# Optimization experiments

Measured on AMD Instinct MI355X. Metric: run time of the kernel, lower is better.

The kernel has to match this reference:

```python
import jax, jax.numpy as jnp
import numpy as np

B, S, D = 2, 400, 512  # batch, seq (src == tgt for self-attention), dim; attn_hidden=0 so d == D


def setup_inputs() -> dict:
    key = jax.random.key(0)
    ks = jax.random.split(key, 9)
    inv = 1.0 / np.sqrt(D)
    return {
        "input": jax.random.normal(ks[0], (B, S, D), jnp.float32),
        "memory_bank": jax.random.normal(ks[1], (B, S, D), jnp.float32),
        # lengths in [S//2, S], guaranteed >= 2 so no row is fully masked
        "memory_lengths": jax.random.randint(ks[2], (B,), S // 2, S + 1, jnp.int32),
        "Wq": jax.random.normal(ks[3], (D, D), jnp.float32) * inv,   # linear_query.weight^T
        "bq": jax.random.normal(ks[4], (D,), jnp.float32) * inv,      # linear_query.bias
        "Wc": jax.random.normal(ks[5], (D, D), jnp.float32) * inv,   # linear_context.weight^T
        "v": jax.random.normal(ks[6], (D,), jnp.float32) * inv,       # v.weight (d -> 1)
        "Wout": jax.random.normal(ks[7], (2 * D, D), jnp.float32) * inv,  # linear_out.weight^T
        "bout": jax.random.normal(ks[8], (D,), jnp.float32) * inv,
    }


def reference(input, memory_bank, memory_lengths, Wq, bq, Wc, v, Wout, bout):
    b, s, d = memory_bank.shape
    # Bahdanau/mlp score: v^T tanh(Wq q + b + Wc h)
    wq = jnp.einsum("btd,de->bte", input, Wq) + bq            # [B,T,d]
    uh = jnp.einsum("bsd,de->bse", memory_bank, Wc)           # [B,S,d]
    wquh = jnp.tanh(wq[:, :, None, :] + uh[:, None, :, :])    # [B,T,S,d] big intermediate
    scores = jnp.einsum("btse,e->bts", wquh, v)               # [B,T,S]
    # padding mask (j < length) with self position masked out on the diagonal
    pos = jnp.arange(s)
    key_mask = pos[None, :] < memory_lengths[:, None]         # [B,S]
    mask = key_mask[:, None, :] & (pos[:, None] != pos[None, :])  # [B,T,S]
    scores = jnp.where(mask, scores, -jnp.inf)
    align = jax.nn.softmax(scores, axis=2)                    # [B,T,S]
    c = jnp.einsum("bts,bsd->btd", align, memory_bank)        # context [B,T,D]
    concat_c = jnp.concatenate([c, input], axis=2)            # [B,T,2D]
    attn_h = jnp.einsum("btf,fd->btd", concat_c, Wout) + bout # [B,T,D]
    # mlp variant: no sigmoid gating
    return attn_h.transpose(1, 0, 2), align.transpose(1, 0, 2)  # [T,B,D], [T,B,S]
```

## Files before the change

kernel.cpp:

```cpp
#include <hip/hip_runtime.h>
#include <math.h>

#define BB 2
#define SS 400
#define DD 512
#define TWO_LOG2E 2.8853900817779268f

#if __has_builtin(__builtin_amdgcn_exp2f)
#define EXP2F(x) __builtin_amdgcn_exp2f(x)
#else
#define EXP2F(x) exp2f(x)
#endif
#define RCPF(x) __builtin_amdgcn_rcpf(x)

#define EAOFF 0
#define MOFF 409600
#define EB4OFF 819200
#define XOFF 1228800

typedef __bf16 bf16x8 __attribute__((ext_vector_type(8)));
typedef float floatx16 __attribute__((ext_vector_type(16)));

__global__ __launch_bounds__(256) void k0_prep(
    const float* __restrict__ Wq, const float* __restrict__ Wc,
    const float* __restrict__ Wout, unsigned short* __restrict__ wt)
{
    const int k0 = blockIdx.x * 32;
    const int n0 = blockIdx.y * 32;
    const int g  = blockIdx.z;

    __shared__ float tile[32][33];
    const int nn  = threadIdx.x & 31;
    const int kk0 = threadIdx.x >> 5;
    const int n   = n0 + nn;

    #pragma unroll
    for (int p = 0; p < 4; ++p) {
        const int k = k0 + kk0 + p * 8;
        float val;
        if (n0 < 512) val = (g ? Wc : Wq)[(size_t)k * 512 + n];
        else          val = Wout[((size_t)(g ? k : 512 + k)) * 512 + (n - 512)];
        tile[kk0 + p * 8][nn] = val;
    }
    __syncthreads();

    const int kc = threadIdx.x & 31;
    #pragma unroll
    for (int p = 0; p < 4; ++p) {
        const int nl = (threadIdx.x >> 5) + p * 8;
        const __bf16 h = (__bf16)tile[kc][nl];
        wt[((size_t)(g * 1024 + n0 + nl)) * 512 + k0 + kc] =
            __builtin_bit_cast(unsigned short, h);
    }
}

__global__ __launch_bounds__(256) void k0b_conv(
    const float* __restrict__ input, const float* __restrict__ mbk,
    unsigned short* __restrict__ ahi, unsigned short* __restrict__ alo)
{
    const int g  = blockIdx.y;
    const int i4 = blockIdx.x * 256 + threadIdx.x;
    const float4 a = ((const float4*)(g ? mbk : input))[i4];
    ushort4 h, l;
    #pragma unroll
    for (int j = 0; j < 4; ++j) {
        const float av = (&a.x)[j];
        const __bf16 hh = (__bf16)av;
        (&h.x)[j] = __builtin_bit_cast(unsigned short, hh);
        const __bf16 ll = (__bf16)(av - (float)hh);
        (&l.x)[j] = __builtin_bit_cast(unsigned short, ll);
    }
    ((ushort4*)(ahi + (size_t)g * 409600))[i4] = h;
    ((ushort4*)(alo + (size_t)g * 409600))[i4] = l;
}

__global__ __launch_bounds__(64) void k1_mfma(
    const unsigned short* __restrict__ ahi, const unsigned short* __restrict__ alo,
    const unsigned short* __restrict__ wt, const float* __restrict__ bq,
    const float* __restrict__ bout, float* __restrict__ ws,
    float* __restrict__ out0)
{
    const int lane = threadIdx.x;
    const int mt   = blockIdx.x;
    const int np   = blockIdx.y;
    const int g    = blockIdx.z;
    const int m    = lane & 31;
    const int kh   = lane >> 5;
    const int n0   = np * 64;

    const size_t arow = ((size_t)g * 800 + mt * 32 + m) * 512 + kh * 8;
    const unsigned short* __restrict__ ah = ahi + arow;
    const unsigned short* __restrict__ al = alo + arow;
    const unsigned short* __restrict__ w0 =
        wt + ((size_t)(g * 1024 + n0 + m)) * 512 + kh * 8;
    const unsigned short* __restrict__ w1 = w0 + (size_t)32 * 512;

    floatx16 acc0h, acc0l, acc1h, acc1l;
    #pragma unroll
    for (int i = 0; i < 16; ++i) { acc0h[i] = 0.f; acc0l[i] = 0.f;
                                   acc1h[i] = 0.f; acc1l[i] = 0.f; }

    #pragma unroll 4
    for (int ks = 0; ks < 32; ++ks) {
        const bf16x8 va0 = *(const bf16x8*)(ah + ks * 16);
        const bf16x8 va1 = *(const bf16x8*)(al + ks * 16);
        const bf16x8 bh0 = *(const bf16x8*)(w0 + ks * 16);
        const bf16x8 bh1 = *(const bf16x8*)(w1 + ks * 16);

        acc0h = __builtin_amdgcn_mfma_f32_32x32x16_bf16(va0, bh0, acc0h, 0, 0, 0);
        acc0l = __builtin_amdgcn_mfma_f32_32x32x16_bf16(va1, bh0, acc0l, 0, 0, 0);
        acc1h = __builtin_amdgcn_mfma_f32_32x32x16_bf16(va0, bh1, acc1h, 0, 0, 0);
        acc1l = __builtin_amdgcn_mfma_f32_32x32x16_bf16(va1, bh1, acc1l, 0, 0, 0);
    }

    const floatx16 c0 = acc0h + acc0l;
    const floatx16 c1 = acc1h + acc1l;
    const int rbase = kh * 4;

    #pragma unroll
    for (int r = 0; r < 16; ++r) {
        const int row  = (r & 3) + 8 * (r >> 2) + rbase;
        const int grow = mt * 32 + row;
        const int bi   = (grow >= SS) ? 1 : 0;
        const int rl   = grow - bi * SS;
        #pragma unroll
        for (int u = 0; u < 2; ++u) {
            const float val  = u ? c1[r] : c0[r];
            const int   gcol = n0 + u * 32 + m;
            if (g == 0) {
                if (gcol < 512) {
                    ws[EAOFF + (size_t)grow * 512 + gcol] =
                        EXP2F(TWO_LOG2E * (val + bq[gcol]));
                } else {
                    const int d = gcol - 512;
                    out0[((size_t)(rl * BB + bi)) * 512 + d] = val + bout[d];
                }
            } else {
                if (gcol < 512) {
                    ws[EB4OFF + (size_t)((bi * 128 + (gcol >> 2)) * SS + rl) * 4
                       + (gcol & 3)] = EXP2F(TWO_LOG2E * val);
                } else {
                    ws[MOFF + (size_t)grow * 512 + (gcol - 512)] = val;
                }
            }
        }
    }
}

__global__ __launch_bounds__(448) void k2_attn(
    const float* __restrict__ ws, const float* __restrict__ v,
    const int* __restrict__ lens, float* __restrict__ out1)
{
    const int tp = blockIdx.x;
    const int b  = blockIdx.y;
    const int t0 = tp * 2;
    const int t1 = t0 + 1;
    const int tid = threadIdx.x;
    const int s   = tid;
    const int sidx = (s < SS) ? s : 0;
    const int len  = lens[b];

    __shared__ float lea[2][512];
    __shared__ float lv[512];
    for (int i = tid; i < 1024; i += 448)
        lea[i >> 9][i & 511] =
            ws[EAOFF + (size_t)(b * SS + t0 + (i >> 9)) * 512 + (i & 511)];
    for (int i = tid; i < 512; i += 448) lv[i] = v[i];
    __syncthreads();

    const float4* __restrict__ eb4 =
        (const float4*)(ws + EB4OFF) + (size_t)b * 128 * SS + sidx;

    float acc0 = 0.f, acc1 = 0.f;
    #pragma unroll 4
    for (int e4 = 0; e4 < 128; ++e4) {
        const float4 eb  = eb4[(size_t)e4 * SS];
        const float4 vv  = *(const float4*)&lv[e4 * 4];
        const float4 ea0 = *(const float4*)&lea[0][e4 * 4];
        const float4 ea1 = *(const float4*)&lea[1][e4 * 4];
        #pragma unroll
        for (int j = 0; j < 4; ++j) {
            const float ebv = (&eb.x)[j];
            const float vj  = (&vv.x)[j];
            acc0 = fmaf(vj, RCPF(fmaf((&ea0.x)[j], ebv, 1.f)), acc0);
            acc1 = fmaf(vj, RCPF(fmaf((&ea1.x)[j], ebv, 1.f)), acc1);
        }
    }

    const bool v0 = (s < SS) && (s < len) && (s != t0);
    const bool v1 = (s < SS) && (s < len) && (s != t1);
    const float sc0 = v0 ? -2.f * acc0 : -INFINITY;
    const float sc1 = v1 ? -2.f * acc1 : -INFINITY;

    __shared__ float wred0[8], wred1[8];
    const int wid  = tid >> 6;
    const int lane = tid & 63;

    float m0 = sc0, m1 = sc1;
    #pragma unroll
    for (int off = 32; off > 0; off >>= 1) {
        m0 = fmaxf(m0, __shfl_xor(m0, off));
        m1 = fmaxf(m1, __shfl_xor(m1, off));
    }
    if (lane == 0) { wred0[wid] = m0; wred1[wid] = m1; }
    __syncthreads();
    float mx0 = wred0[0], mx1 = wred1[0];
    #pragma unroll
    for (int w = 1; w < 7; ++w) {
        mx0 = fmaxf(mx0, wred0[w]);
        mx1 = fmaxf(mx1, wred1[w]);
    }
    __syncthreads();

    const float p0 = v0 ? __expf(sc0 - mx0) : 0.f;
    const float p1 = v1 ? __expf(sc1 - mx1) : 0.f;
    float s0v = p0, s1v = p1;
    #pragma unroll
    for (int off = 32; off > 0; off >>= 1) {
        s0v += __shfl_xor(s0v, off);
        s1v += __shfl_xor(s1v, off);
    }
    if (lane == 0) { wred0[wid] = s0v; wred1[wid] = s1v; }
    __syncthreads();
    float tot0 = wred0[0], tot1 = wred1[0];
    #pragma unroll
    for (int w = 1; w < 7; ++w) { tot0 += wred0[w]; tot1 += wred1[w]; }
    const float inv0 = RCPF(tot0);
    const float inv1 = RCPF(tot1);

    if (s < SS) {
        out1[((size_t)(t0 * BB) + b) * SS + s] = p0 * inv0;
        out1[((size_t)(t1 * BB) + b) * SS + s] = p1 * inv1;
    }
}

__global__ __launch_bounds__(256) void k3_out(
    const float* __restrict__ ws, const float* __restrict__ align_out,
    float* __restrict__ out0)
{
    const int d     = blockIdx.x * 256 + threadIdx.x;
    const int r0    = blockIdx.y * 4;
    const int b     = (r0 >= SS) ? 1 : 0;
    const int tbase = r0 - b * SS;

    const float* __restrict__ Mb = ws + MOFF + (size_t)b * SS * DD;

    float pv[4];
    #pragma unroll
    for (int j = 0; j < 4; ++j)
        pv[j] = out0[((size_t)((tbase + j) * BB) + b) * DD + d];

    float acc[4];
    #pragma unroll
    for (int j = 0; j < 4; ++j) acc[j] = 0.f;

    float mA[4], mB[4];
    float4 alA[4], alB[4];

    auto LOAD = [&](float (&mm)[4], float4 (&al)[4], int s) {
        #pragma unroll
        for (int i = 0; i < 4; ++i)
            mm[i] = Mb[(size_t)(s + i) * DD + d];
        #pragma unroll
        for (int j = 0; j < 4; ++j)
            al[j] = *(const float4*)(align_out +
                     ((size_t)((tbase + j) * BB) + b) * SS + s);
    };
    auto FMA4 = [&](const float (&mm)[4], const float4 (&al)[4]) {
        #pragma unroll
        for (int j = 0; j < 4; ++j) {
            acc[j] = fmaf(al[j].x, mm[0], acc[j]);
            acc[j] = fmaf(al[j].y, mm[1], acc[j]);
            acc[j] = fmaf(al[j].z, mm[2], acc[j]);
            acc[j] = fmaf(al[j].w, mm[3], acc[j]);
        }
    };

    LOAD(mA, alA, 0);
    for (int s = 0; s < SS; s += 8) {
        LOAD(mB, alB, s + 4);
        FMA4(mA, alA);
        if (s + 8 < SS) LOAD(mA, alA, s + 8);
        FMA4(mB, alB);
    }

    #pragma unroll
    for (int j = 0; j < 4; ++j)
        out0[((size_t)((tbase + j) * BB) + b) * DD + d] = acc[j] + pv[j];
}

extern "C" void kernel_launch(void* const* d_in, const int* in_sizes, int n_in,
                              void* d_out, int out_size, void* d_ws, size_t ws_size,
                              hipStream_t stream)
{
    const float* input = (const float*)d_in[0];
    const float* mbk   = (const float*)d_in[1];
    const int*   lens  = (const int*)d_in[2];
    const float* Wq    = (const float*)d_in[3];
    const float* bq    = (const float*)d_in[4];
    const float* Wc    = (const float*)d_in[5];
    const float* v     = (const float*)d_in[6];
    const float* Wout  = (const float*)d_in[7];
    const float* bout  = (const float*)d_in[8];

    float* out0 = (float*)d_out;
    float* out1 = out0 + (size_t)BB * SS * DD;
    float* ws   = (float*)d_ws;
    unsigned short* x16 = (unsigned short*)(ws + XOFF);
    unsigned short* wt  = x16;
    unsigned short* ahi = x16 + 1048576;
    unsigned short* alo = ahi + 819200;

    hipLaunchKernelGGL(k0_prep, dim3(16, 32, 2), dim3(256), 0, stream,
                       Wq, Wc, Wout, wt);
    hipLaunchKernelGGL(k0b_conv, dim3(400, 2), dim3(256), 0, stream,
                       input, mbk, ahi, alo);
    hipLaunchKernelGGL(k1_mfma, dim3(25, 16, 2), dim3(64), 0, stream,
                       ahi, alo, wt, bq, bout, ws, out0);
    hipLaunchKernelGGL(k2_attn, dim3(200, 2), dim3(448), 0, stream,
                       ws, v, lens, out1);
    hipLaunchKernelGGL(k3_out, dim3(2, 200), dim3(256), 0, stream,
                       ws, out1, out0);
}
```

Baseline: 157.0 us.

## Fuse prep kernels and merge attention softmax with context output

Merges the weight-transpose and activation-split kernels into one launch, and fuses the attention score/softmax kernel with the context/output accumulation kernel. Each attention block now handles four query rows instead of two and keeps the alignment weights in shared memory, so the separate pass that re-reads them from global memory goes away. The trade-offs are a grid of only 200 blocks of 512 threads, which may underfill the GPU, and a serial 400-step loop per thread in the output stage.

```diff
diff --git a/kernel.cpp b/kernel.cpp
--- a/kernel.cpp
+++ b/kernel.cpp
@@ -21,57 +21,59 @@
 typedef __bf16 bf16x8 __attribute__((ext_vector_type(8)));
 typedef float floatx16 __attribute__((ext_vector_type(16)));
 
-__global__ __launch_bounds__(256) void k0_prep(
+__global__ __launch_bounds__(256) void k0_all(
     const float* __restrict__ Wq, const float* __restrict__ Wc,
-    const float* __restrict__ Wout, unsigned short* __restrict__ wt)
-{
-    const int k0 = blockIdx.x * 32;
-    const int n0 = blockIdx.y * 32;
-    const int g  = blockIdx.z;
-
-    __shared__ float tile[32][33];
-    const int nn  = threadIdx.x & 31;
-    const int kk0 = threadIdx.x >> 5;
-    const int n   = n0 + nn;
-
-    #pragma unroll
-    for (int p = 0; p < 4; ++p) {
-        const int k = k0 + kk0 + p * 8;
-        float val;
-        if (n0 < 512) val = (g ? Wc : Wq)[(size_t)k * 512 + n];
-        else          val = Wout[((size_t)(g ? k : 512 + k)) * 512 + (n - 512)];
-        tile[kk0 + p * 8][nn] = val;
-    }
-    __syncthreads();
-
-    const int kc = threadIdx.x & 31;
-    #pragma unroll
-    for (int p = 0; p < 4; ++p) {
-        const int nl = (threadIdx.x >> 5) + p * 8;
-        const __bf16 h = (__bf16)tile[kc][nl];
-        wt[((size_t)(g * 1024 + n0 + nl)) * 512 + k0 + kc] =
-            __builtin_bit_cast(unsigned short, h);
-    }
-}
-
-__global__ __launch_bounds__(256) void k0b_conv(
-    const float* __restrict__ input, const float* __restrict__ mbk,
+    const float* __restrict__ Wout, const float* __restrict__ input,
+    const float* __restrict__ mbk, unsigned short* __restrict__ wt,
     unsigned short* __restrict__ ahi, unsigned short* __restrict__ alo)
 {
-    const int g  = blockIdx.y;
-    const int i4 = blockIdx.x * 256 + threadIdx.x;
-    const float4 a = ((const float4*)(g ? mbk : input))[i4];
-    ushort4 h, l;
-    #pragma unroll
-    for (int j = 0; j < 4; ++j) {
-        const float av = (&a.x)[j];
-        const __bf16 hh = (__bf16)av;
-        (&h.x)[j] = __builtin_bit_cast(unsigned short, hh);
-        const __bf16 ll = (__bf16)(av - (float)hh);
-        (&l.x)[j] = __builtin_bit_cast(unsigned short, ll);
-    }
-    ((ushort4*)(ahi + (size_t)g * 409600))[i4] = h;
-    ((ushort4*)(alo + (size_t)g * 409600))[i4] = l;
+    const int gid = blockIdx.x;
+    if (gid < 1024) {
+        const int g   = gid >> 9;
+        const int rem = gid & 511;
+        const int k0  = (rem & 15) * 32;
+        const int n0  = (rem >> 4) * 32;
+
+        __shared__ float tile[32][33];
+        const int nn  = threadIdx.x & 31;
+        const int kk0 = threadIdx.x >> 5;
+        const int n   = n0 + nn;
+
+        #pragma unroll
+        for (int p = 0; p < 4; ++p) {
+            const int k = k0 + kk0 + p * 8;
+            float val;
+            if (n0 < 512) val = (g ? Wc : Wq)[(size_t)k * 512 + n];
+            else          val = Wout[((size_t)(g ? k : 512 + k)) * 512 + (n - 512)];
+            tile[kk0 + p * 8][nn] = val;
+        }
+        __syncthreads();
+
+        const int kc = threadIdx.x & 31;
+        #pragma unroll
+        for (int p = 0; p < 4; ++p) {
+            const int nl = (threadIdx.x >> 5) + p * 8;
+            const __bf16 h = (__bf16)tile[kc][nl];
+            wt[((size_t)(g * 1024 + n0 + nl)) * 512 + k0 + kc] =
+                __builtin_bit_cast(unsigned short, h);
+        }
+    } else {
+        const int cid = gid - 1024;
+        const int g   = (cid >= 400) ? 1 : 0;
+        const int i4  = (cid - g * 400) * 256 + threadIdx.x;
+        const float4 a = ((const float4*)(g ? mbk : input))[i4];
+        ushort4 h, l;
+        #pragma unroll
+        for (int j = 0; j < 4; ++j) {
+            const float av = (&a.x)[j];
+            const __bf16 hh = (__bf16)av;
+            (&h.x)[j] = __builtin_bit_cast(unsigned short, hh);
+            const __bf16 ll = (__bf16)(av - (float)hh);
+            (&l.x)[j] = __builtin_bit_cast(unsigned short, ll);
+        }
+        ((ushort4*)(ahi + (size_t)g * 409600))[i4] = h;
+        ((ushort4*)(alo + (size_t)g * 409600))[i4] = l;
+    }
 }
 
 __global__ __launch_bounds__(64) void k1_mfma(
@@ -147,146 +149,138 @@
     }
 }
 
-__global__ __launch_bounds__(448) void k2_attn(
+__global__ __launch_bounds__(512) void k23_attn(
     const float* __restrict__ ws, const float* __restrict__ v,
-    const int* __restrict__ lens, float* __restrict__ out1)
+    const int* __restrict__ lens, float* __restrict__ out1,
+    float* __restrict__ out0)
 {
-    const int tp = blockIdx.x;
+    const int tq = blockIdx.x;
     const int b  = blockIdx.y;
-    const int t0 = tp * 2;
-    const int t1 = t0 + 1;
+    const int t0 = tq * 4;
     const int tid = threadIdx.x;
     const int s   = tid;
     const int sidx = (s < SS) ? s : 0;
     const int len  = lens[b];
 
-    __shared__ float lea[2][512];
+    __shared__ float lea[4][512];
     __shared__ float lv[512];
-    for (int i = tid; i < 1024; i += 448)
+    __shared__ float al4[SS][4];
+    __shared__ float wred[4][8];
+
+    for (int i = tid; i < 2048; i += 512)
         lea[i >> 9][i & 511] =
             ws[EAOFF + (size_t)(b * SS + t0 + (i >> 9)) * 512 + (i & 511)];
-    for (int i = tid; i < 512; i += 448) lv[i] = v[i];
+    lv[tid] = v[tid];
     __syncthreads();
 
     const float4* __restrict__ eb4 =
         (const float4*)(ws + EB4OFF) + (size_t)b * 128 * SS + sidx;
 
-    float acc0 = 0.f, acc1 = 0.f;
+    float acc[4] = {0.f, 0.f, 0.f, 0.f};
     #pragma unroll 4
     for (int e4 = 0; e4 < 128; ++e4) {
         const float4 eb  = eb4[(size_t)e4 * SS];
         const float4 vv  = *(const float4*)&lv[e4 * 4];
         const float4 ea0 = *(const float4*)&lea[0][e4 * 4];
         const float4 ea1 = *(const float4*)&lea[1][e4 * 4];
+        const float4 ea2 = *(const float4*)&lea[2][e4 * 4];
+        const float4 ea3 = *(const float4*)&lea[3][e4 * 4];
         #pragma unroll
         for (int j = 0; j < 4; ++j) {
             const float ebv = (&eb.x)[j];
             const float vj  = (&vv.x)[j];
-            acc0 = fmaf(vj, RCPF(fmaf((&ea0.x)[j], ebv, 1.f)), acc0);
-            acc1 = fmaf(vj, RCPF(fmaf((&ea1.x)[j], ebv, 1.f)), acc1);
-        }
-    }
-
-    const bool v0 = (s < SS) && (s < len) && (s != t0);
-    const bool v1 = (s < SS) && (s < len) && (s != t1);
-    const float sc0 = v0 ? -2.f * acc0 : -INFINITY;
-    const float sc1 = v1 ? -2.f * acc1 : -INFINITY;
-
-    __shared__ float wred0[8], wred1[8];
+            acc[0] = fmaf(vj, RCPF(fmaf((&ea0.x)[j], ebv, 1.f)), acc[0]);
+            acc[1] = fmaf(vj, RCPF(fmaf((&ea1.x)[j], ebv, 1.f)), acc[1]);
+            acc[2] = fmaf(vj, RCPF(fmaf((&ea2.x)[j], ebv, 1.f)), acc[2]);
+            acc[3] = fmaf(vj, RCPF(fmaf((&ea3.x)[j], ebv, 1.f)), acc[3]);
+        }
+    }
+
+    bool  vmask[4];
+    float sc[4];
+    #pragma unroll
+    for (int t = 0; t < 4; ++t) {
+        vmask[t] = (s < SS) && (s < len) && (s != t0 + t);
+        sc[t] = vmask[t] ? -2.f * acc[t] : -INFINITY;
+    }
+
     const int wid  = tid >> 6;
     const int lane = tid & 63;
 
-    float m0 = sc0, m1 = sc1;
+    float mloc[4] = {sc[0], sc[1], sc[2], sc[3]};
     #pragma unroll
     for (int off = 32; off > 0; off >>= 1) {
-        m0 = fmaxf(m0, __shfl_xor(m0, off));
-        m1 = fmaxf(m1, __shfl_xor(m1, off));
-    }
-    if (lane == 0) { wred0[wid] = m0; wred1[wid] = m1; }
-    __syncthreads();
-    float mx0 = wred0[0], mx1 = wred1[0];
-    #pragma unroll
-    for (int w = 1; w < 7; ++w) {
-        mx0 = fmaxf(mx0, wred0[w]);
-        mx1 = fmaxf(mx1, wred1[w]);
-    }
-    __syncthreads();
-
-    const float p0 = v0 ? __expf(sc0 - mx0) : 0.f;
-    const float p1 = v1 ? __expf(sc1 - mx1) : 0.f;
-    float s0v = p0, s1v = p1;
+        #pragma unroll
+        for (int t = 0; t < 4; ++t)
+            mloc[t] = fmaxf(mloc[t], __shfl_xor(mloc[t], off));
+    }
+    if (lane == 0) {
+        #pragma unroll
+        for (int t = 0; t < 4; ++t) wred[t][wid] = mloc[t];
+    }
+    __syncthreads();
+    float mx[4];
+    #pragma unroll
+    for (int t = 0; t < 4; ++t) {
+        float m = wred[t][0];
+        #pragma unroll
+        for (int w = 1; w < 8; ++w) m = fmaxf(m, wred[t][w]);
+        mx[t] = m;
+    }
+    __syncthreads();
+
+    float p[4], sloc[4];
+    #pragma unroll
+    for (int t = 0; t < 4; ++t) {
+        p[t] = vmask[t] ? __expf(sc[t] - mx[t]) : 0.f;
+        sloc[t] = p[t];
+    }
     #pragma unroll
     for (int off = 32; off > 0; off >>= 1) {
-        s0v += __shfl_xor(s0v, off);
-        s1v += __shfl_xor(s1v, off);
-    }
-    if (lane == 0) { wred0[wid] = s0v; wred1[wid] = s1v; }
-    __syncthreads();
-    float tot0 = wred0[0], tot1 = wred1[0];
-    #pragma unroll
-    for (int w = 1; w < 7; ++w) { tot0 += wred0[w]; tot1 += wred1[w]; }
-    const float inv0 = RCPF(tot0);
-    const float inv1 = RCPF(tot1);
-
-    if (s < SS) {
-        out1[((size_t)(t0 * BB) + b) * SS + s] = p0 * inv0;
-        out1[((size_t)(t1 * BB) + b) * SS + s] = p1 * inv1;
-    }
-}
-
-__global__ __launch_bounds__(256) void k3_out(
-    const float* __restrict__ ws, const float* __restrict__ align_out,
-    float* __restrict__ out0)
-{
-    const int d     = blockIdx.x * 256 + threadIdx.x;
-    const int r0    = blockIdx.y * 4;
-    const int b     = (r0 >= SS) ? 1 : 0;
-    const int tbase = r0 - b * SS;
-
+        #pragma unroll
+        for (int t = 0; t < 4; ++t) sloc[t] += __shfl_xor(sloc[t], off);
+    }
+    if (lane == 0) {
+        #pragma unroll
+        for (int t = 0; t < 4; ++t) wred[t][wid] = sloc[t];
+    }
+    __syncthreads();
+    #pragma unroll
+    for (int t = 0; t < 4; ++t) {
+        float tot = wred[t][0];
+        #pragma unroll
+        for (int w = 1; w < 8; ++w) tot += wred[t][w];
+        const float a = p[t] * RCPF(tot);
+        if (s < SS) {
+            out1[((size_t)((t0 + t) * BB) + b) * SS + s] = a;
+            al4[s][t] = a;
+        }
+    }
+    __syncthreads();
+
+    const int d = tid;
     const float* __restrict__ Mb = ws + MOFF + (size_t)b * SS * DD;
 
-    float pv[4];
-    #pragma unroll
-    for (int j = 0; j < 4; ++j)
-        pv[j] = out0[((size_t)((tbase + j) * BB) + b) * DD + d];
-
-    float acc[4];
-    #pragma unroll
-    for (int j = 0; j < 4; ++j) acc[j] = 0.f;
-
-    float mA[4], mB[4];
-    float4 alA[4], alB[4];
-
-    auto LOAD = [&](float (&mm)[4], float4 (&al)[4], int s) {
-        #pragma unroll
-        for (int i = 0; i < 4; ++i)
-            mm[i] = Mb[(size_t)(s + i) * DD + d];
-        #pragma unroll
-        for (int j = 0; j < 4; ++j)
-            al[j] = *(const float4*)(align_out +
-                     ((size_t)((tbase + j) * BB) + b) * SS + s);
-    };
-    auto FMA4 = [&](const float (&mm)[4], const float4 (&al)[4]) {
-        #pragma unroll
-        for (int j = 0; j < 4; ++j) {
-            acc[j] = fmaf(al[j].x, mm[0], acc[j]);
-            acc[j] = fmaf(al[j].y, mm[1], acc[j]);
-            acc[j] = fmaf(al[j].z, mm[2], acc[j]);
-            acc[j] = fmaf(al[j].w, mm[3], acc[j]);
-        }
-    };
-
-    LOAD(mA, alA, 0);
-    for (int s = 0; s < SS; s += 8) {
-        LOAD(mB, alB, s + 4);
-        FMA4(mA, alA);
-        if (s + 8 < SS) LOAD(mA, alA, s + 8);
-        FMA4(mB, alB);
-    }
-
-    #pragma unroll
-    for (int j = 0; j < 4; ++j)
-        out0[((size_t)((tbase + j) * BB) + b) * DD + d] = acc[j] + pv[j];
+    float pv[4], oacc[4];
+    #pragma unroll
+    for (int t = 0; t < 4; ++t) {
+        pv[t]   = out0[((size_t)((t0 + t) * BB) + b) * DD + d];
+        oacc[t] = 0.f;
+    }
+
+    #pragma unroll 4
+    for (int ss = 0; ss < SS; ++ss) {
+        const float  mv = Mb[(size_t)ss * DD + d];
+        const float4 a4 = *(const float4*)&al4[ss][0];
+        oacc[0] = fmaf((&a4.x)[0], mv, oacc[0]);
+        oacc[1] = fmaf((&a4.x)[1], mv, oacc[1]);
+        oacc[2] = fmaf((&a4.x)[2], mv, oacc[2]);
+        oacc[3] = fmaf((&a4.x)[3], mv, oacc[3]);
+    }
+
+    #pragma unroll
+    for (int t = 0; t < 4; ++t)
+        out0[((size_t)((t0 + t) * BB) + b) * DD + d] = oacc[t] + pv[t];
 }
 
 extern "C" void kernel_launch(void* const* d_in, const int* in_sizes, int n_in,
@@ -311,14 +305,10 @@
     unsigned short* ahi = x16 + 1048576;
     unsigned short* alo = ahi + 819200;
 
-    hipLaunchKernelGGL(k0_prep, dim3(16, 32, 2), dim3(256), 0, stream,
-                       Wq, Wc, Wout, wt);
-    hipLaunchKernelGGL(k0b_conv, dim3(400, 2), dim3(256), 0, stream,
-                       input, mbk, ahi, alo);
+    hipLaunchKernelGGL(k0_all, dim3(1824), dim3(256), 0, stream,
+                       Wq, Wc, Wout, input, mbk, wt, ahi, alo);
     hipLaunchKernelGGL(k1_mfma, dim3(25, 16, 2), dim3(64), 0, stream,
                        ahi, alo, wt, bq, bout, ws, out0);
-    hipLaunchKernelGGL(k2_attn, dim3(200, 2), dim3(448), 0, stream,
-                       ws, v, lens, out1);
-    hipLaunchKernelGGL(k3_out, dim3(2, 200), dim3(256), 0, stream,
-                       ws, out1, out0);
+    hipLaunchKernelGGL(k23_attn, dim3(100, 2), dim3(512), 0, stream,
+                       ws, v, lens, out1, out0);
 }
```

After: 171.6 us. +9.3%, slower.
